# Kernel tuning notes

Hardware: AMD Instinct MI355X
Metric: run time of the kernel (lower is better)

The kernel has to match this reference:

```python
import jax, jax.numpy as jnp
import numpy as np

B, N, C = 4, 2048, 512
H = 8
HD = C // H  # 64
SCALE = HD ** -0.5


def setup_inputs() -> dict:
    key = jax.random.key(0)
    k1, k2, k3 = jax.random.split(key, 3)
    x = jax.random.normal(k1, (B, N, C), dtype=jnp.float32)
    w_qkv = jax.random.normal(k2, (3 * C, C), dtype=jnp.float32) * (C ** -0.5)
    b_qkv = jnp.zeros((3 * C,), dtype=jnp.float32)
    w_proj = jax.random.normal(k3, (C, C), dtype=jnp.float32) * (C ** -0.5)
    b_proj = jnp.zeros((C,), dtype=jnp.float32)
    return {"x": x, "w_qkv": w_qkv, "b_qkv": b_qkv, "w_proj": w_proj, "b_proj": b_proj}


def reference(x, w_qkv, b_qkv, w_proj, b_proj):
    # qkv projection: (B,N,C) @ (C,3C) -> (B,N,3,H,HD) -> (3,B,H,N,HD)
    qkv = (x @ w_qkv.T + b_qkv).reshape(B, N, 3, H, HD).transpose(2, 0, 3, 1, 4)
    q, k, v = qkv[0], qkv[1], qkv[2]
    # scores (B,H,N,N), scale applied after matmul as in the torch source
    attn = jnp.einsum('bhnd,bhmd->bhnm', q, k) * SCALE
    attn = jax.nn.softmax(attn, axis=-1)
    out = jnp.einsum('bhnm,bhmd->bhnd', attn, v)  # (B,H,N,HD)
    out = out.transpose(0, 2, 1, 3).reshape(B, N, C)
    return out @ w_proj.T + b_proj
```

## Files before the change

kernel.cpp:

```cpp
#include <hip/hip_runtime.h>

#define B_ 4
#define N_ 2048
#define C_ 512
#define H_ 8
#define HD_ 64
#define SCALE_ 0.125f
#define QSCALE_ 0.18033688011112042f

typedef __attribute__((ext_vector_type(8))) __bf16 bf16x8;
typedef __attribute__((ext_vector_type(4))) float f32x4;
typedef __attribute__((ext_vector_type(4))) unsigned int u32x4;
typedef __attribute__((ext_vector_type(2))) unsigned int u32x2;
typedef __attribute__((ext_vector_type(4))) short s16x4;

#if __has_builtin(__builtin_amdgcn_mfma_f32_16x16x16bf16_1k)
#define MFMA16(acc, a, b) acc = __builtin_amdgcn_mfma_f32_16x16x16bf16_1k(a, b, acc, 0, 0, 0)
#else
#define MFMA16(acc, a, b) \
    asm("v_mfma_f32_16x16x16_bf16 %0, %1, %2, %0" : "+v"(acc) : "v"(a), "v"(b))
#endif

__device__ __forceinline__ unsigned short f2bf(float f) {
    unsigned int u = __builtin_bit_cast(unsigned int, f);
    u += 0x7fffu + ((u >> 16) & 1u);
    return (unsigned short)(u >> 16);
}

__device__ __forceinline__ void llds16(const void* g, void* l) {
    __builtin_amdgcn_global_load_lds(
        (const __attribute__((address_space(1))) unsigned int*)g,
        (__attribute__((address_space(3))) unsigned int*)l, 16, 0, 0);
}

__global__ __launch_bounds__(256) void cvt_all(const float* __restrict__ x,
                                               const float* __restrict__ wq,
                                               const float* __restrict__ wp,
                                               unsigned short* __restrict__ xb,
                                               unsigned short* __restrict__ wqb,
                                               unsigned short* __restrict__ wpb) {
    const int NX = B_ * N_ * C_ / 4, NQ = 3 * C_ * C_ / 4, NP = C_ * C_ / 4;
    int i = blockIdx.x * 256 + threadIdx.x;
    const float4* src;
    ushort4* dst;
    int idx;
    if (i < NX) { src = (const float4*)x; dst = (ushort4*)xb; idx = i; }
    else if (i < NX + NQ) { src = (const float4*)wq; dst = (ushort4*)wqb; idx = i - NX; }
    else if (i < NX + NQ + NP) { src = (const float4*)wp; dst = (ushort4*)wpb; idx = i - NX - NQ; }
    else return;
    float4 v = src[idx];
    ushort4 o;
    o.x = f2bf(v.x); o.y = f2bf(v.y); o.z = f2bf(v.z); o.w = f2bf(v.w);
    dst[idx] = o;
}

template <int MODE>
__global__ __launch_bounds__(256) void gemm_bt(const unsigned short* __restrict__ A,
                                               const unsigned short* __restrict__ Bw,
                                               const float* __restrict__ bias,
                                               float* __restrict__ Out,
                                               unsigned short* __restrict__ Qb,
                                               unsigned short* __restrict__ Kb,
                                               unsigned short* __restrict__ Vt) {
    constexpr int K = 512;
    __shared__ __align__(16) unsigned char smem[32768];
    unsigned char* sA = smem;
    unsigned char* sB = smem + 16384;

    const int tid = threadIdx.x;
    const int lane = tid & 63;
    const int wave = tid >> 6;
    const int wm = wave >> 1, wn = wave & 1;
    const int m0 = blockIdx.y * 128;
    const int n0 = blockIdx.x * 128;

    f32x4 acc[4][4] = {};

    for (int k0 = 0; k0 < K; k0 += 64) {
#pragma unroll
        for (int i = 0; i < 4; i++) {
            int ci = wave * 4 + i;
            int row = ci * 8 + (lane >> 3);
            int cb = (lane & 7) * 16;
            const unsigned char* ga =
                (const unsigned char*)A + ((size_t)(m0 + row) * K + k0) * 2 + cb;
            const unsigned char* gb =
                (const unsigned char*)Bw + ((size_t)(n0 + row) * K + k0) * 2 + cb;
            llds16(ga, sA + ci * 1024);
            llds16(gb, sB + ci * 1024);
        }
        __syncthreads();
#pragma unroll
        for (int kk = 0; kk < 2; kk++) {
            bf16x8 af[4], bfr[4];
#pragma unroll
            for (int mi = 0; mi < 4; mi++)
                af[mi] = *(const bf16x8*)(sA + (wm * 64 + mi * 16 + (lane & 15)) * 128 +
                                          kk * 64 + (lane >> 4) * 16);
#pragma unroll
            for (int ni = 0; ni < 4; ni++)
                bfr[ni] = *(const bf16x8*)(sB + (wn * 64 + ni * 16 + (lane & 15)) * 128 +
                                           kk * 64 + (lane >> 4) * 16);
#pragma unroll
            for (int mi = 0; mi < 4; mi++)
#pragma unroll
                for (int ni = 0; ni < 4; ni++)
                    acc[mi][ni] = __builtin_amdgcn_mfma_f32_16x16x32_bf16(
                        af[mi], bfr[ni], acc[mi][ni], 0, 0, 0);
        }
        __syncthreads();
    }

    if constexpr (MODE == 0) {
#pragma unroll
        for (int ni = 0; ni < 4; ni++) {
            int c = n0 + wn * 64 + ni * 16 + (lane & 15);
            int sel = c >> 9, h = (c >> 6) & 7, d = c & 63;
            float bv = bias[c];
#pragma unroll
            for (int mi = 0; mi < 4; mi++) {
#pragma unroll
                for (int r = 0; r < 4; r++) {
                    int m = m0 + wm * 64 + mi * 16 + ((lane >> 4) << 2) + r;
                    int b = m >> 11, n = m & (N_ - 1);
                    float fv = acc[mi][ni][r] + bv;
                    if (sel == 0) {
                        Qb[((size_t)(b * H_ + h) * N_ + n) * HD_ + d] = f2bf(fv * QSCALE_);
                    } else if (sel == 1) {
                        Kb[((size_t)(b * H_ + h) * N_ + n) * HD_ + d] = f2bf(fv);
                    } else {
                        Vt[((size_t)(b * H_ + h) * HD_ + d) * (size_t)N_ + n] = f2bf(fv);
                    }
                }
            }
        }
    } else {
#pragma unroll
        for (int ni = 0; ni < 4; ni++) {
            int c = n0 + wn * 64 + ni * 16 + (lane & 15);
            float bv = bias[c];
#pragma unroll
            for (int mi = 0; mi < 4; mi++) {
#pragma unroll
                for (int r = 0; r < 4; r++) {
                    int m = m0 + wm * 64 + mi * 16 + ((lane >> 4) << 2) + r;
                    Out[(size_t)m * C_ + c] = acc[mi][ni][r] + bv;
                }
            }
        }
    }
}

__global__ __launch_bounds__(512, 4) void attn_fwd(const unsigned short* __restrict__ Qb,
                                                   const unsigned short* __restrict__ Kb,
                                                   const unsigned short* __restrict__ Vt,
                                                   unsigned short* __restrict__ AO) {
    __shared__ __align__(16) unsigned char smem[32768];

    const int tid = threadIdx.x, lane = tid & 63, wave = tid >> 6;
    const int g = lane >> 4, c = lane & 15;
    const int bh = blockIdx.y;
    const int q0 = blockIdx.x * 128 + wave * 16;
    const unsigned short* Qh = Qb + (size_t)bh * N_ * HD_;
    const unsigned short* Kh = Kb + (size_t)bh * N_ * HD_;
    const unsigned short* Vh = Vt + (size_t)bh * HD_ * N_;

    bf16x8 qf[2];
#pragma unroll
    for (int kk = 0; kk < 2; kk++)
        qf[kk] = *(const bf16x8*)(Qh + (size_t)(q0 + c) * HD_ + kk * 32 + g * 8);

    s16x4 ones16;
#pragma unroll
    for (int i = 0; i < 4; i++) ones16[i] = (short)0x3F80;

    f32x4 o[4] = {};
    f32x4 osum = {};

    const int srow = tid >> 3;
    const int sslot = (tid & 7) * 16;
    const int ssw = (sslot ^ ((srow & 7) << 4));

    {
        u32x4 kreg = *(const u32x4*)((const unsigned char*)Kh + (size_t)srow * 128 + sslot);
        u32x4 vreg = *(const u32x4*)((const unsigned char*)Vh + (size_t)srow * (N_ * 2) + sslot);
        *(u32x4*)(smem + srow * 128 + ssw) = kreg;
        *(u32x4*)(smem + 16384 + srow * 128 + ssw) = vreg;
    }
    __syncthreads();

#pragma unroll 1
    for (int t = 0; t < N_ / 64; t++) {
        unsigned char* bK = smem + (t & 1) * 8192;
        unsigned char* bV = smem + 16384 + (t & 1) * 8192;

        u32x4 kreg, vreg;
        if (t < N_ / 64 - 1) {
            int kv0 = (t + 1) * 64;
            kreg = *(const u32x4*)((const unsigned char*)Kh + (size_t)(kv0 + srow) * 128 + sslot);
            vreg = *(const u32x4*)((const unsigned char*)Vh + (size_t)srow * (N_ * 2) +
                                   kv0 * 2 + sslot);
        }

        f32x4 s[4] = {};
#pragma unroll
        for (int j = 0; j < 4; j++) {
#pragma unroll
            for (int kk = 0; kk < 2; kk++) {
                int krow = j * 16 + c;
                bf16x8 kf = *(const bf16x8*)(bK + krow * 128 +
                                             ((kk * 64 + g * 16) ^ ((krow & 7) << 4)));
                s[j] = __builtin_amdgcn_mfma_f32_16x16x32_bf16(kf, qf[kk], s[j], 0, 0, 0);
            }
        }

        s16x4 pa[4];
#pragma unroll
        for (int j = 0; j < 4; j++) {
            float p0 = __builtin_exp2f(s[j][0]);
            float p1 = __builtin_exp2f(s[j][1]);
            float p2 = __builtin_exp2f(s[j][2]);
            float p3 = __builtin_exp2f(s[j][3]);
            unsigned int lo, hi;
            asm("v_cvt_pk_bf16_f32 %0, %1, %2" : "=v"(lo) : "v"(p0), "v"(p1));
            asm("v_cvt_pk_bf16_f32 %0, %1, %2" : "=v"(hi) : "v"(p2), "v"(p3));
            u32x2 w;
            w[0] = lo;
            w[1] = hi;
            pa[j] = __builtin_bit_cast(s16x4, w);
        }

#pragma unroll
        for (int j = 0; j < 4; j++) {
            MFMA16(osum, pa[j], ones16);
#pragma unroll
            for (int dj = 0; dj < 4; dj++) {
                int vrow = dj * 16 + c;
                u32x2 vv = *(const u32x2*)(bV + vrow * 128 +
                                           ((j * 32 + 8 * g) ^ ((vrow & 7) << 4)));
                s16x4 vfj = __builtin_bit_cast(s16x4, vv);
                MFMA16(o[dj], pa[j], vfj);
            }
        }

        if (t < N_ / 64 - 1) {
            unsigned char* nK = smem + ((t + 1) & 1) * 8192;
            unsigned char* nV = smem + 16384 + ((t + 1) & 1) * 8192;
            *(u32x4*)(nK + srow * 128 + ssw) = kreg;
            *(u32x4*)(nV + srow * 128 + ssw) = vreg;
        }
        __syncthreads();
    }

    const int b = bh >> 3, h = bh & 7;
#pragma unroll
    for (int r = 0; r < 4; r++) {
        float inv = 1.0f / osum[r];
        int n = q0 + (g << 2) + r;
#pragma unroll
        for (int dj = 0; dj < 4; dj++) {
            int col = h * HD_ + dj * 16 + c;
            AO[((size_t)(b * N_ + n)) * C_ + col] = f2bf(o[dj][r] * inv);
        }
    }
}

extern "C" void kernel_launch(void* const* d_in, const int* in_sizes, int n_in,
                              void* d_out, int out_size, void* d_ws, size_t ws_size,
                              hipStream_t stream) {
    const float* x = (const float*)d_in[0];
    const float* w_qkv = (const float*)d_in[1];
    const float* b_qkv = (const float*)d_in[2];
    const float* w_proj = (const float*)d_in[3];
    const float* b_proj = (const float*)d_in[4];
    float* out = (float*)d_out;

    unsigned char* ws = (unsigned char*)d_ws;
    unsigned short* xb = (unsigned short*)ws;
    unsigned short* AO = xb;
    unsigned short* wqb = (unsigned short*)(ws + 8388608);
    unsigned short* wpb = (unsigned short*)(ws + 8388608 + 1572864);
    unsigned short* Vt = (unsigned short*)(ws + 8388608 + 1572864 + 524288);

    unsigned short* Qb = (unsigned short*)d_out;
    unsigned short* Kb = Qb + (size_t)B_ * H_ * N_ * HD_;

    const int NALL = (B_ * N_ * C_ + 3 * C_ * C_ + C_ * C_) / 4;
    cvt_all<<<(NALL + 255) / 256, 256, 0, stream>>>(x, w_qkv, w_proj, xb, wqb, wpb);

    gemm_bt<0><<<dim3(12, 64), 256, 0, stream>>>(xb, wqb, b_qkv, nullptr, Qb, Kb, Vt);
    attn_fwd<<<dim3(16, 32), 512, 0, stream>>>(Qb, Kb, Vt, AO);
    gemm_bt<1><<<dim3(4, 64), 256, 0, stream>>>(AO, wpb, b_proj, out, nullptr, nullptr, nullptr);
}
```

Measured before the change: 131.6 us.

## Stage V-transpose epilogue through swizzled LDS and remap attention block order

In the QKV GEMM epilogue, tiles that produce V are first written to shared memory with an XOR swizzle, then read back and stored to the transposed Vt layout as 16-byte vector writes. This replaces scattered 2-byte stores with a large stride. Q/K tiles now choose their destination once per block instead of branching per element. The attention kernel also remaps its linear block index so consecutive blocks cover different (batch, head) pairs, which changes cache locality across the grid and relies on the grid being 16 wide.

```diff
diff --git a/kernel.cpp b/kernel.cpp
--- a/kernel.cpp
+++ b/kernel.cpp
@@ -112,24 +112,52 @@
     }
 
     if constexpr (MODE == 0) {
-#pragma unroll
-        for (int ni = 0; ni < 4; ni++) {
-            int c = n0 + wn * 64 + ni * 16 + (lane & 15);
-            int sel = c >> 9, h = (c >> 6) & 7, d = c & 63;
-            float bv = bias[c];
-#pragma unroll
-            for (int mi = 0; mi < 4; mi++) {
-#pragma unroll
-                for (int r = 0; r < 4; r++) {
-                    int m = m0 + wm * 64 + mi * 16 + ((lane >> 4) << 2) + r;
-                    int b = m >> 11, n = m & (N_ - 1);
-                    float fv = acc[mi][ni][r] + bv;
-                    if (sel == 0) {
-                        Qb[((size_t)(b * H_ + h) * N_ + n) * HD_ + d] = f2bf(fv * QSCALE_);
-                    } else if (sel == 1) {
-                        Kb[((size_t)(b * H_ + h) * N_ + n) * HD_ + d] = f2bf(fv);
-                    } else {
-                        Vt[((size_t)(b * H_ + h) * HD_ + d) * (size_t)N_ + n] = f2bf(fv);
+        if (n0 >= 1024) {
+            unsigned char* T = smem;
+#pragma unroll
+            for (int ni = 0; ni < 4; ni++) {
+                int cl = wn * 64 + ni * 16 + (lane & 15);
+                float bv = bias[n0 + cl];
+#pragma unroll
+                for (int mi = 0; mi < 4; mi++) {
+#pragma unroll
+                    for (int r = 0; r < 4; r++) {
+                        int ml = wm * 64 + mi * 16 + ((lane >> 4) << 2) + r;
+                        *(unsigned short*)(T + cl * 256 + ((ml * 2) ^ ((cl & 7) << 4))) =
+                            f2bf(acc[mi][ni][r] + bv);
+                    }
+                }
+            }
+            __syncthreads();
+            const int b = m0 >> 11;
+#pragma unroll
+            for (int it = 0; it < 8; it++) {
+                int li = it * 256 + tid;
+                int cl2 = li >> 4, mc = li & 15;
+                int cg = n0 + cl2;
+                int h = (cg >> 6) & 7, d = cg & 63;
+                u32x4 vv = *(const u32x4*)(T + cl2 * 256 + ((mc * 16) ^ ((cl2 & 7) << 4)));
+                int n = (m0 & (N_ - 1)) + mc * 8;
+                *(u32x4*)((unsigned char*)Vt +
+                          (((size_t)(b * H_ + h) * HD_ + d) * N_ + n) * 2) = vv;
+            }
+        } else {
+            const bool selq = (n0 < 512);
+#pragma unroll
+            for (int ni = 0; ni < 4; ni++) {
+                int cg = n0 + wn * 64 + ni * 16 + (lane & 15);
+                int h = (cg >> 6) & 7, d = cg & 63;
+                float bv = bias[cg];
+#pragma unroll
+                for (int mi = 0; mi < 4; mi++) {
+#pragma unroll
+                    for (int r = 0; r < 4; r++) {
+                        int m = m0 + wm * 64 + mi * 16 + ((lane >> 4) << 2) + r;
+                        int b = m >> 11, n = m & (N_ - 1);
+                        float fv = acc[mi][ni][r] + bv;
+                        size_t idx = ((size_t)(b * H_ + h) * N_ + n) * HD_ + d;
+                        if (selq) Qb[idx] = f2bf(fv * QSCALE_);
+                        else Kb[idx] = f2bf(fv);
                     }
                 }
             }
@@ -159,8 +187,10 @@
 
     const int tid = threadIdx.x, lane = tid & 63, wave = tid >> 6;
     const int g = lane >> 4, c = lane & 15;
-    const int bh = blockIdx.y;
-    const int q0 = blockIdx.x * 128 + wave * 16;
+    const int L = blockIdx.y * 16 + blockIdx.x;
+    const int bh = (L & 7) * 4 + ((L >> 3) & 3);
+    const int qx = L >> 5;
+    const int q0 = qx * 128 + wave * 16;
     const unsigned short* Qh = Qb + (size_t)bh * N_ * HD_;
     const unsigned short* Kh = Kb + (size_t)bh * N_ * HD_;
     const unsigned short* Vh = Vt + (size_t)bh * HD_ * N_;
```

Result: faster. 112.1 us (-14.8%).
